# Performance work log

Measured on AMD Instinct MI355X. Metric: run time of the kernel, lower is better.

The kernel has to match this reference:

```python
import jax, jax.numpy as jnp
import numpy as np

N_NODES = 50000
N_EDGES = 800000
H, D_IN, D_OUT = 4, 256, 64


def setup_inputs() -> dict:
    key = jax.random.key(0)
    ks = jax.random.split(key, 7)
    x = jax.random.normal(ks[0], (N_NODES, D_IN), dtype=jnp.float32)
    idx = jax.random.randint(ks[1], (2, N_EDGES), 0, N_NODES, dtype=jnp.int32)
    elem = jax.random.uniform(ks[2], (N_EDGES,), dtype=jnp.float32)
    Ws = jax.random.normal(ks[3], (H, D_IN, D_OUT), dtype=jnp.float32) * 0.05
    bs = jax.random.normal(ks[4], (H, D_OUT), dtype=jnp.float32) * 0.05
    aw = jax.random.normal(ks[5], (H, 2 * D_OUT + 1), dtype=jnp.float32) * 0.05
    ab = jax.random.normal(ks[6], (H,), dtype=jnp.float32) * 0.05
    return {"x": x, "idx": idx, "elem": elem, "Ws": Ws, "bs": bs, "aw": aw, "ab": ab}


def reference(x, idx, elem, Ws, bs, aw, ab):
    N = x.shape[0]
    O = Ws.shape[-1]
    # per-head MLP (num_mlp_layers=1 -> single Linear): [H, N, O]
    feats = jnp.einsum('nd,hdo->hno', x, Ws) + bs[:, None, :]
    # attention linear on concat(src, dst, elem): split weights instead of
    # materializing the [E, 2O+1] concat; math is identical.
    aw_src, aw_dst, aw_e = aw[:, :O], aw[:, O:2 * O], aw[:, 2 * O]
    a_s = jnp.einsum('hno,ho->hn', feats, aw_src)   # [H, N]
    a_d = jnp.einsum('hno,ho->hn', feats, aw_dst)   # [H, N]
    src, dst = idx[0], idx[1]
    score = a_s[:, src] + a_d[:, dst] + aw_e[:, None] * elem[None, :] + ab[:, None]
    w = jnp.exp(-jax.nn.relu(score / 20.0))        # [H, E], in (0, 1]
    dst_f = feats[:, dst]                          # [H, E, O] gather
    seg = lambda vals: jax.ops.segment_sum(vals, src, num_segments=N)
    pooled = jax.vmap(lambda wi, fi: seg(wi[:, None] * fi))(w, dst_f)  # [H, N, O]
    row_sum = jax.vmap(lambda wi: seg(wi))(w)                          # [H, N]
    out = pooled / row_sum[:, :, None]
    # concat heads along feature dim: [N, H*O]
    return jnp.transpose(out, (1, 0, 2)).reshape(N, H * O)
```

## Files before the change

kernel.cpp:

```cpp
#include <hip/hip_runtime.h>
#include <math.h>

constexpr int DIN = 256;
constexpr int H   = 4;
constexpr int O   = 64;
constexpr int HO  = H * O;
constexpr int AWS = 2 * O + 1;

typedef __bf16 bf16x8 __attribute__((ext_vector_type(8)));
typedef float  f32x4  __attribute__((ext_vector_type(4)));

__device__ __forceinline__ float bf2f(unsigned short u) {
    union { unsigned int i; float f; } c;
    c.i = ((unsigned int)u) << 16;
    return c.f;
}

__global__ __launch_bounds__(256) void k_prep_hist(const float* __restrict__ Ws,
    __bf16* __restrict__ Bt, const int* __restrict__ idx, int E,
    int* __restrict__ cnt, int* __restrict__ rank)
{
    const int b = blockIdx.x;
    if (b < 256) {
        const int i = b * 256 + threadIdx.x;
        const int k = i & 255;
        const int n = i >> 8;
        Bt[n * 256 + k] = (__bf16)Ws[(n >> 6) * (DIN * O) + k * O + (n & 63)];
    } else {
        const int e = (b - 256) * 256 + threadIdx.x;
        if (e < E) rank[e] = atomicAdd(&cnt[idx[e]], 1);
    }
}

__global__ __launch_bounds__(256) void k_gemm(const float* __restrict__ x,
    const __bf16* __restrict__ Bt, const float* __restrict__ bs,
    const float* __restrict__ aw, int N,
    __bf16* __restrict__ F, float* __restrict__ a_sT, float* __restrict__ a_dT)
{
    __shared__ __bf16 As[64][DIN + 8];
    const int t    = threadIdx.x;
    const int w    = t >> 6;
    const int lane = t & 63;
    const int c15  = lane & 15;
    const int quad = lane >> 4;
    const int n0   = blockIdx.x * 64;

    #pragma unroll
    for (int i = 0; i < 16; ++i) {
        const int r   = i * 4 + w;
        const int row = n0 + r;
        float4 xv = make_float4(0.f, 0.f, 0.f, 0.f);
        if (row < N) xv = *(const float4*)&x[(size_t)row * DIN + lane * 4];
        __bf16* dst = &As[r][lane * 4];
        dst[0] = (__bf16)xv.x; dst[1] = (__bf16)xv.y;
        dst[2] = (__bf16)xv.z; dst[3] = (__bf16)xv.w;
    }
    __syncthreads();

    f32x4 acc[4][4] = {};
    const __bf16* BtW = Bt + (size_t)(w * 64) * 256;
    const int kq = quad * 8;

    #pragma unroll
    for (int k0 = 0; k0 < DIN; k0 += 32) {
        bf16x8 afr[4], bfr[4];
        #pragma unroll
        for (int rt = 0; rt < 4; ++rt)
            afr[rt] = *(const bf16x8*)&As[rt * 16 + c15][k0 + kq];
        #pragma unroll
        for (int ct = 0; ct < 4; ++ct)
            bfr[ct] = *(const bf16x8*)&BtW[(size_t)(ct * 16 + c15) * 256 + k0 + kq];
        #pragma unroll
        for (int rt = 0; rt < 4; ++rt)
            #pragma unroll
            for (int ct = 0; ct < 4; ++ct)
                acc[rt][ct] = __builtin_amdgcn_mfma_f32_16x16x32_bf16(
                    afr[rt], bfr[ct], acc[rt][ct], 0, 0, 0);
    }

    const int h = w;
    float bsv[4], awsv[4], awdv[4];
    #pragma unroll
    for (int ct = 0; ct < 4; ++ct) {
        const int col = ct * 16 + c15;
        bsv[ct]  = bs[w * 64 + col];
        awsv[ct] = aw[h * AWS + col];
        awdv[ct] = aw[h * AWS + O + col];
    }

    #pragma unroll
    for (int rt = 0; rt < 4; ++rt) {
        float psum[4] = {0.f, 0.f, 0.f, 0.f};
        float pdum[4] = {0.f, 0.f, 0.f, 0.f};
        #pragma unroll
        for (int ct = 0; ct < 4; ++ct) {
            #pragma unroll
            for (int reg = 0; reg < 4; ++reg) {
                const float f = acc[rt][ct][reg] + bsv[ct];
                const int row = n0 + rt * 16 + quad * 4 + reg;
                if (row < N)
                    F[(size_t)row * HO + w * 64 + ct * 16 + c15] = (__bf16)f;
                psum[reg] = fmaf(f, awsv[ct], psum[reg]);
                pdum[reg] = fmaf(f, awdv[ct], pdum[reg]);
            }
        }
        #pragma unroll
        for (int reg = 0; reg < 4; ++reg) {
            float v = psum[reg], u = pdum[reg];
            #pragma unroll
            for (int off = 1; off < 16; off <<= 1) {
                v += __shfl_xor(v, off, 64);
                u += __shfl_xor(u, off, 64);
            }
            const int row = n0 + rt * 16 + quad * 4 + reg;
            if (c15 == 0 && row < N) {
                a_sT[row * H + h] = v;
                a_dT[row * H + h] = u;
            }
        }
    }
}

__global__ __launch_bounds__(256) void k_scan1(const int* __restrict__ cnt,
    int* __restrict__ row_ptr, int* __restrict__ bsum, int N)
{
    __shared__ int wsum[4], woff[4];
    const int t = threadIdx.x, b = blockIdx.x;
    const int i = b * 256 + t;
    const int lane = t & 63, w = t >> 6;

    const int v = (i < N) ? cnt[i] : 0;
    int s = v;
    #pragma unroll
    for (int off = 1; off < 64; off <<= 1) {
        int u = __shfl_up(s, off, 64);
        if (lane >= off) s += u;
    }
    if (lane == 63) wsum[w] = s;
    __syncthreads();
    if (t == 0) {
        int run = 0;
        #pragma unroll
        for (int j = 0; j < 4; ++j) { woff[j] = run; run += wsum[j]; }
        bsum[b] = run;
    }
    __syncthreads();
    if (i < N) row_ptr[i] = s - v + woff[w];
}

__global__ __launch_bounds__(256) void k_scan2(int* __restrict__ bsum, int nb)
{
    __shared__ int wsum[4], woff[4];
    const int t = threadIdx.x;
    const int lane = t & 63, w = t >> 6;

    const int v = (t < nb) ? bsum[t] : 0;
    int s = v;
    #pragma unroll
    for (int off = 1; off < 64; off <<= 1) {
        int u = __shfl_up(s, off, 64);
        if (lane >= off) s += u;
    }
    if (lane == 63) wsum[w] = s;
    __syncthreads();
    if (t == 0) {
        int run = 0;
        #pragma unroll
        for (int j = 0; j < 4; ++j) { woff[j] = run; run += wsum[j]; }
    }
    __syncthreads();
    const int excl = s - v + woff[w];
    __syncthreads();
    if (t < nb) bsum[t] = excl;
    if (t == 0) bsum[nb] = woff[3] + wsum[3];
}

__global__ __launch_bounds__(256) void k_scan3(int* __restrict__ row_ptr,
    const int* __restrict__ bsum, int N, int nb)
{
    const int b = blockIdx.x;
    const int i = b * 256 + threadIdx.x;
    if (i < N) row_ptr[i] += bsum[b];
    if (b == 0 && threadIdx.x == 0) row_ptr[N] = bsum[nb];
}

__global__ __launch_bounds__(256) void k_scatter(const int* __restrict__ idx,
    const float* __restrict__ elem, const int* __restrict__ rank,
    const int* __restrict__ row_ptr, int E, int2* __restrict__ csr)
{
    int e = blockIdx.x * 256 + threadIdx.x;
    if (e >= E) return;
    const int s = idx[e];
    const int d = idx[E + e];
    const int pos = row_ptr[s] + rank[e];
    csr[pos] = make_int2(d, __float_as_int(elem[e]));
}

__global__ __launch_bounds__(256) void k_gather(const int* __restrict__ row_ptr,
    const int2* __restrict__ csr, const float* __restrict__ a_sT,
    const float* __restrict__ a_dT, const float* __restrict__ aw,
    const float* __restrict__ ab, const __bf16* __restrict__ F,
    float* __restrict__ out, int N)
{
    __shared__ int2  s_rec[4][64];
    __shared__ float s_w[4][256];
    __shared__ int   s_cw[4];

    const int t    = threadIdx.x;
    const int wv   = t >> 6;
    const int lane = t & 63;
    const int n    = blockIdx.x * 4 + wv;
    const int h16  = lane >> 4;
    const int h4   = lane & 3;

    int beg = 0, deg = 0;
    if (n < N) { beg = row_ptr[n]; deg = row_ptr[n + 1] - beg; }
    const int cw = (deg + 63) >> 6;
    if (lane == 0) s_cw[wv] = cw;
    __syncthreads();
    const int maxc = max(max(s_cw[0], s_cw[1]), max(s_cw[2], s_cw[3]));

    const float asv = (n < N) ? a_sT[n * H + h4] : 0.f;
    const float awe = aw[h4 * AWS + 2 * O];
    const float abv = ab[h4];

    float4 acc = make_float4(0.f, 0.f, 0.f, 0.f);
    float  rs  = 0.f;

    for (int p = 0; p < maxc; ++p) {
        const int base = beg + p * 64;
        const int cnt  = min(64, deg - p * 64);
        const bool act = (p < cw);
        __syncthreads();
        if (act && lane < cnt) s_rec[wv][lane] = csr[base + lane];
        __syncthreads();
        if (act) {
            for (int v = lane; v < cnt * 4; v += 64) {
                const int j = v >> 2;
                const int2 r = s_rec[wv][j];
                const float el = __int_as_float(r.y);
                const float score = asv + a_dT[r.x * H + h4] + awe * el + abv;
                s_w[wv][j * 4 + h4] = __expf(-fmaxf(score * 0.05f, 0.f));
            }
        }
        __syncthreads();
        if (act) {
            for (int j = 0; j < cnt; ++j) {
                const int d = s_rec[wv][j].x;
                const float w = s_w[wv][j * 4 + h16];
                const ushort4 fv = *(const ushort4*)&F[(size_t)d * HO + lane * 4];
                acc.x = fmaf(w, bf2f(fv.x), acc.x);
                acc.y = fmaf(w, bf2f(fv.y), acc.y);
                acc.z = fmaf(w, bf2f(fv.z), acc.z);
                acc.w = fmaf(w, bf2f(fv.w), acc.w);
                rs += w;
            }
        }
    }

    if (n < N) {
        const float inv = 1.f / rs;
        float4 o = make_float4(acc.x * inv, acc.y * inv, acc.z * inv, acc.w * inv);
        *(float4*)&out[(size_t)n * HO + lane * 4] = o;
    }
}

extern "C" void kernel_launch(void* const* d_in, const int* in_sizes, int n_in,
                              void* d_out, int out_size, void* d_ws, size_t ws_size,
                              hipStream_t stream)
{
    const float* x    = (const float*)d_in[0];
    const int*   idx  = (const int*)d_in[1];
    const float* elem = (const float*)d_in[2];
    const float* Ws   = (const float*)d_in[3];
    const float* bs   = (const float*)d_in[4];
    const float* aw   = (const float*)d_in[5];
    const float* ab   = (const float*)d_in[6];

    const int N = in_sizes[0] / DIN;
    const int E = in_sizes[1] / 2;
    const int nb = (N + 255) / 256;

    __bf16* F      = (__bf16*)d_ws;
    float* a_sT    = (float*)(F + (size_t)N * HO);
    float* a_dT    = a_sT + (size_t)N * H;
    int*   cnt     = (int*)(a_dT + (size_t)N * H);
    int*   row_ptr = cnt + N;
    int*   rank    = row_ptr + (N + 1);
    int*   bsum    = rank + E;
    size_t off = (size_t)((char*)(bsum + nb + 1) - (char*)d_ws);
    off = (off + 7) & ~(size_t)7;
    int2*  csr     = (int2*)((char*)d_ws + off);
    __bf16* Bt     = (__bf16*)(csr + E);
    float* out     = (float*)d_out;

    hipMemsetAsync(cnt, 0, (size_t)N * sizeof(int), stream);

    k_prep_hist<<<256 + (E + 255) / 256, 256, 0, stream>>>(Ws, Bt, idx, E, cnt, rank);
    k_gemm<<<(N + 63) / 64, 256, 0, stream>>>(x, Bt, bs, aw, N, F, a_sT, a_dT);
    k_scan1<<<nb, 256, 0, stream>>>(cnt, row_ptr, bsum, N);
    k_scan2<<<1, 256, 0, stream>>>(bsum, nb);
    k_scan3<<<nb, 256, 0, stream>>>(row_ptr, bsum, N, nb);
    k_scatter<<<(E + 255) / 256, 256, 0, stream>>>(idx, elem, rank, row_ptr, E, csr);
    k_gather<<<(N + 3) / 4, 256, 0, stream>>>(row_ptr, csr, a_sT, a_dT, aw, ab,
                                              F, out, N);
}
```

Before: 277.6 us.

## Fuse histogram into GEMM launch, drop scan3, and streamline per-wave gather

Replaces the memset with a zeroing branch in the prep kernel and moves the edge histogram atomics into extra blocks of the GEMM launch. It removes the third scan pass by adding block offsets at use sites in scatter and gather. The gather kernel drops block-wide barriers, so each wave processes its own node independently. It computes all four head weights per edge with vector loads and unrolls the feature accumulation by four. The per-wave shared-memory handoff now relies only on a block fence rather than barriers.

```diff
diff --git a/kernel.cpp b/kernel.cpp
--- a/kernel.cpp
+++ b/kernel.cpp
@@ -8,6 +8,7 @@
 constexpr int AWS = 2 * O + 1;
 
 typedef __bf16 bf16x8 __attribute__((ext_vector_type(8)));
+typedef __bf16 bf16x4 __attribute__((ext_vector_type(4)));
 typedef float  f32x4  __attribute__((ext_vector_type(4)));
 
 __device__ __forceinline__ float bf2f(unsigned short u) {
@@ -16,9 +17,8 @@
     return c.f;
 }
 
-__global__ __launch_bounds__(256) void k_prep_hist(const float* __restrict__ Ws,
-    __bf16* __restrict__ Bt, const int* __restrict__ idx, int E,
-    int* __restrict__ cnt, int* __restrict__ rank)
+__global__ __launch_bounds__(256) void k_prep(const float* __restrict__ Ws,
+    __bf16* __restrict__ Bt, int* __restrict__ cnt, int N)
 {
     const int b = blockIdx.x;
     if (b < 256) {
@@ -27,23 +27,37 @@
         const int n = i >> 8;
         Bt[n * 256 + k] = (__bf16)Ws[(n >> 6) * (DIN * O) + k * O + (n & 63)];
     } else {
-        const int e = (b - 256) * 256 + threadIdx.x;
-        if (e < E) rank[e] = atomicAdd(&cnt[idx[e]], 1);
-    }
-}
-
-__global__ __launch_bounds__(256) void k_gemm(const float* __restrict__ x,
+        const int i = (b - 256) * 256 + threadIdx.x;
+        if (i < N) cnt[i] = 0;
+    }
+}
+
+__global__ __launch_bounds__(256) void k_gemm_hist(const float* __restrict__ x,
     const __bf16* __restrict__ Bt, const float* __restrict__ bs,
-    const float* __restrict__ aw, int N,
-    __bf16* __restrict__ F, float* __restrict__ a_sT, float* __restrict__ a_dT)
+    const float* __restrict__ aw, int N, int GB,
+    __bf16* __restrict__ F, float* __restrict__ a_sT, float* __restrict__ a_dT,
+    const int* __restrict__ idx, int E, int* __restrict__ cnt,
+    int* __restrict__ rank)
 {
     __shared__ __bf16 As[64][DIN + 8];
-    const int t    = threadIdx.x;
+    const int b = blockIdx.x;
+    const int t = threadIdx.x;
+
+    if (b >= GB) {
+        const int base_e = (b - GB) * 1024 + t;
+        #pragma unroll
+        for (int i = 0; i < 4; ++i) {
+            const int e = base_e + i * 256;
+            if (e < E) rank[e] = atomicAdd(&cnt[idx[e]], 1);
+        }
+        return;
+    }
+
     const int w    = t >> 6;
     const int lane = t & 63;
     const int c15  = lane & 15;
     const int quad = lane >> 4;
-    const int n0   = blockIdx.x * 64;
+    const int n0   = b * 64;
 
     #pragma unroll
     for (int i = 0; i < 16; ++i) {
@@ -51,9 +65,8 @@
         const int row = n0 + r;
         float4 xv = make_float4(0.f, 0.f, 0.f, 0.f);
         if (row < N) xv = *(const float4*)&x[(size_t)row * DIN + lane * 4];
-        __bf16* dst = &As[r][lane * 4];
-        dst[0] = (__bf16)xv.x; dst[1] = (__bf16)xv.y;
-        dst[2] = (__bf16)xv.z; dst[3] = (__bf16)xv.w;
+        bf16x4 pv = { (__bf16)xv.x, (__bf16)xv.y, (__bf16)xv.z, (__bf16)xv.w };
+        *(bf16x4*)&As[r][lane * 4] = pv;
     }
     __syncthreads();
 
@@ -145,7 +158,9 @@
         bsum[b] = run;
     }
     __syncthreads();
-    if (i < N) row_ptr[i] = s - v + woff[w];
+    const int excl = s - v + woff[w];
+    if (i < N) row_ptr[i] = excl;
+    if (i == N - 1) row_ptr[N] = excl + v;
 }
 
 __global__ __launch_bounds__(256) void k_scan2(int* __restrict__ bsum, int nb)
@@ -175,94 +190,110 @@
     if (t == 0) bsum[nb] = woff[3] + wsum[3];
 }
 
-__global__ __launch_bounds__(256) void k_scan3(int* __restrict__ row_ptr,
-    const int* __restrict__ bsum, int N, int nb)
-{
-    const int b = blockIdx.x;
-    const int i = b * 256 + threadIdx.x;
-    if (i < N) row_ptr[i] += bsum[b];
-    if (b == 0 && threadIdx.x == 0) row_ptr[N] = bsum[nb];
-}
-
 __global__ __launch_bounds__(256) void k_scatter(const int* __restrict__ idx,
     const float* __restrict__ elem, const int* __restrict__ rank,
-    const int* __restrict__ row_ptr, int E, int2* __restrict__ csr)
+    const int* __restrict__ row_ptr, const int* __restrict__ bsum, int E,
+    int2* __restrict__ csr)
 {
     int e = blockIdx.x * 256 + threadIdx.x;
     if (e >= E) return;
     const int s = idx[e];
     const int d = idx[E + e];
-    const int pos = row_ptr[s] + rank[e];
+    const int pos = row_ptr[s] + bsum[s >> 8] + rank[e];
     csr[pos] = make_int2(d, __float_as_int(elem[e]));
 }
 
 __global__ __launch_bounds__(256) void k_gather(const int* __restrict__ row_ptr,
-    const int2* __restrict__ csr, const float* __restrict__ a_sT,
-    const float* __restrict__ a_dT, const float* __restrict__ aw,
-    const float* __restrict__ ab, const __bf16* __restrict__ F,
-    float* __restrict__ out, int N)
+    const int* __restrict__ bsum, const int2* __restrict__ csr,
+    const float* __restrict__ a_sT, const float* __restrict__ a_dT,
+    const float* __restrict__ aw, const float* __restrict__ ab,
+    const __bf16* __restrict__ F, float* __restrict__ out, int N)
 {
     __shared__ int2  s_rec[4][64];
     __shared__ float s_w[4][256];
-    __shared__ int   s_cw[4];
 
     const int t    = threadIdx.x;
     const int wv   = t >> 6;
     const int lane = t & 63;
     const int n    = blockIdx.x * 4 + wv;
+    if (n >= N) return;
     const int h16  = lane >> 4;
-    const int h4   = lane & 3;
-
-    int beg = 0, deg = 0;
-    if (n < N) { beg = row_ptr[n]; deg = row_ptr[n + 1] - beg; }
-    const int cw = (deg + 63) >> 6;
-    if (lane == 0) s_cw[wv] = cw;
-    __syncthreads();
-    const int maxc = max(max(s_cw[0], s_cw[1]), max(s_cw[2], s_cw[3]));
-
-    const float asv = (n < N) ? a_sT[n * H + h4] : 0.f;
-    const float awe = aw[h4 * AWS + 2 * O];
-    const float abv = ab[h4];
+
+    const int beg = row_ptr[n]     + bsum[n >> 8];
+    const int end = row_ptr[n + 1] + bsum[(n + 1) >> 8];
+
+    const float4 as4 = *(const float4*)&a_sT[n * 4];
+    const float4 ab4 = *(const float4*)&ab[0];
+    const float4 awe4 = make_float4(aw[0 * AWS + 2 * O], aw[1 * AWS + 2 * O],
+                                    aw[2 * AWS + 2 * O], aw[3 * AWS + 2 * O]);
 
     float4 acc = make_float4(0.f, 0.f, 0.f, 0.f);
     float  rs  = 0.f;
-
-    for (int p = 0; p < maxc; ++p) {
-        const int base = beg + p * 64;
-        const int cnt  = min(64, deg - p * 64);
-        const bool act = (p < cw);
-        __syncthreads();
-        if (act && lane < cnt) s_rec[wv][lane] = csr[base + lane];
-        __syncthreads();
-        if (act) {
-            for (int v = lane; v < cnt * 4; v += 64) {
-                const int j = v >> 2;
-                const int2 r = s_rec[wv][j];
-                const float el = __int_as_float(r.y);
-                const float score = asv + a_dT[r.x * H + h4] + awe * el + abv;
-                s_w[wv][j * 4 + h4] = __expf(-fmaxf(score * 0.05f, 0.f));
-            }
-        }
-        __syncthreads();
-        if (act) {
-            for (int j = 0; j < cnt; ++j) {
-                const int d = s_rec[wv][j].x;
-                const float w = s_w[wv][j * 4 + h16];
-                const ushort4 fv = *(const ushort4*)&F[(size_t)d * HO + lane * 4];
-                acc.x = fmaf(w, bf2f(fv.x), acc.x);
-                acc.y = fmaf(w, bf2f(fv.y), acc.y);
-                acc.z = fmaf(w, bf2f(fv.z), acc.z);
-                acc.w = fmaf(w, bf2f(fv.w), acc.w);
-                rs += w;
-            }
-        }
-    }
-
-    if (n < N) {
-        const float inv = 1.f / rs;
-        float4 o = make_float4(acc.x * inv, acc.y * inv, acc.z * inv, acc.w * inv);
-        *(float4*)&out[(size_t)n * HO + lane * 4] = o;
-    }
+    const __bf16* __restrict__ Fl = F + lane * 4;
+
+    for (int base = beg; base < end; base += 64) {
+        const int cnt = min(64, end - base);
+        if (lane < cnt) {
+            const int2 r = csr[base + lane];
+            s_rec[wv][lane] = r;
+            const float el = __int_as_float(r.y);
+            const float4 ad = *(const float4*)&a_dT[r.x * 4];
+            float4 w4;
+            w4.x = __expf(-fmaxf((as4.x + ad.x + awe4.x * el + ab4.x) * 0.05f, 0.f));
+            w4.y = __expf(-fmaxf((as4.y + ad.y + awe4.y * el + ab4.y) * 0.05f, 0.f));
+            w4.z = __expf(-fmaxf((as4.z + ad.z + awe4.z * el + ab4.z) * 0.05f, 0.f));
+            w4.w = __expf(-fmaxf((as4.w + ad.w + awe4.w * el + ab4.w) * 0.05f, 0.f));
+            *(float4*)&s_w[wv][lane * 4] = w4;
+        }
+        __threadfence_block();
+
+        int j = 0;
+        for (; j + 4 <= cnt; j += 4) {
+            const int d0 = s_rec[wv][j + 0].x;
+            const int d1 = s_rec[wv][j + 1].x;
+            const int d2 = s_rec[wv][j + 2].x;
+            const int d3 = s_rec[wv][j + 3].x;
+            const float w0 = s_w[wv][(j + 0) * 4 + h16];
+            const float w1 = s_w[wv][(j + 1) * 4 + h16];
+            const float w2 = s_w[wv][(j + 2) * 4 + h16];
+            const float w3 = s_w[wv][(j + 3) * 4 + h16];
+            const ushort4 f0 = *(const ushort4*)&Fl[(size_t)d0 * HO];
+            const ushort4 f1 = *(const ushort4*)&Fl[(size_t)d1 * HO];
+            const ushort4 f2 = *(const ushort4*)&Fl[(size_t)d2 * HO];
+            const ushort4 f3 = *(const ushort4*)&Fl[(size_t)d3 * HO];
+            acc.x = fmaf(w0, bf2f(f0.x), acc.x);
+            acc.y = fmaf(w0, bf2f(f0.y), acc.y);
+            acc.z = fmaf(w0, bf2f(f0.z), acc.z);
+            acc.w = fmaf(w0, bf2f(f0.w), acc.w);
+            acc.x = fmaf(w1, bf2f(f1.x), acc.x);
+            acc.y = fmaf(w1, bf2f(f1.y), acc.y);
+            acc.z = fmaf(w1, bf2f(f1.z), acc.z);
+            acc.w = fmaf(w1, bf2f(f1.w), acc.w);
+            acc.x = fmaf(w2, bf2f(f2.x), acc.x);
+            acc.y = fmaf(w2, bf2f(f2.y), acc.y);
+            acc.z = fmaf(w2, bf2f(f2.z), acc.z);
+            acc.w = fmaf(w2, bf2f(f2.w), acc.w);
+            acc.x = fmaf(w3, bf2f(f3.x), acc.x);
+            acc.y = fmaf(w3, bf2f(f3.y), acc.y);
+            acc.z = fmaf(w3, bf2f(f3.z), acc.z);
+            acc.w = fmaf(w3, bf2f(f3.w), acc.w);
+            rs += w0 + w1 + w2 + w3;
+        }
+        for (; j < cnt; ++j) {
+            const int d = s_rec[wv][j].x;
+            const float w = s_w[wv][j * 4 + h16];
+            const ushort4 fv = *(const ushort4*)&Fl[(size_t)d * HO];
+            acc.x = fmaf(w, bf2f(fv.x), acc.x);
+            acc.y = fmaf(w, bf2f(fv.y), acc.y);
+            acc.z = fmaf(w, bf2f(fv.z), acc.z);
+            acc.w = fmaf(w, bf2f(fv.w), acc.w);
+            rs += w;
+        }
+    }
+
+    const float inv = 1.f / rs;
+    float4 o = make_float4(acc.x * inv, acc.y * inv, acc.z * inv, acc.w * inv);
+    *(float4*)&out[(size_t)n * HO + lane * 4] = o;
 }
 
 extern "C" void kernel_launch(void* const* d_in, const int* in_sizes, int n_in,
@@ -280,6 +311,8 @@
     const int N = in_sizes[0] / DIN;
     const int E = in_sizes[1] / 2;
     const int nb = (N + 255) / 256;
+    const int GB = (N + 63) / 64;
+    const int HB = (E + 1023) / 1024;
 
     __bf16* F      = (__bf16*)d_ws;
     float* a_sT    = (float*)(F + (size_t)N * HO);
@@ -294,14 +327,13 @@
     __bf16* Bt     = (__bf16*)(csr + E);
     float* out     = (float*)d_out;
 
-    hipMemsetAsync(cnt, 0, (size_t)N * sizeof(int), stream);
-
-    k_prep_hist<<<256 + (E + 255) / 256, 256, 0, stream>>>(Ws, Bt, idx, E, cnt, rank);
-    k_gemm<<<(N + 63) / 64, 256, 0, stream>>>(x, Bt, bs, aw, N, F, a_sT, a_dT);
+    k_prep<<<256 + nb, 256, 0, stream>>>(Ws, Bt, cnt, N);
+    k_gemm_hist<<<GB + HB, 256, 0, stream>>>(x, Bt, bs, aw, N, GB,
+                                             F, a_sT, a_dT, idx, E, cnt, rank);
     k_scan1<<<nb, 256, 0, stream>>>(cnt, row_ptr, bsum, N);
     k_scan2<<<1, 256, 0, stream>>>(bsum, nb);
-    k_scan3<<<nb, 256, 0, stream>>>(row_ptr, bsum, N, nb);
-    k_scatter<<<(E + 255) / 256, 256, 0, stream>>>(idx, elem, rank, row_ptr, E, csr);
-    k_gather<<<(N + 3) / 4, 256, 0, stream>>>(row_ptr, csr, a_sT, a_dT, aw, ab,
-                                              F, out, N);
-}
+    k_scatter<<<(E + 255) / 256, 256, 0, stream>>>(idx, elem, rank, row_ptr,
+                                                   bsum, E, csr);
+    k_gather<<<(N + 3) / 4, 256, 0, stream>>>(row_ptr, bsum, csr, a_sT, a_dT,
+                                              aw, ab, F, out, N);
+}
```

Result: faster. 251.3 us (-9.5%).
